# Performance work log

Measured on AMD Instinct MI355X. Metric: run time of the kernel, lower is better.

## Reference

```python
import jax, jax.numpy as jnp
import numpy as np
import math

D_MODEL, H, D_FF = 1024, 16, 4096
B, S = 4, 2048
EPS = 1e-6

def layer_norm(x, alpha, beta):
    # Faithful to torch: x.std uses Bessel correction (ddof=1), eps added to std.
    mean = jnp.mean(x, axis=-1, keepdims=True)
    std = jnp.std(x, axis=-1, keepdims=True, ddof=1)
    return alpha * (x - mean) / (std + EPS) + beta

def setup_inputs() -> dict:
    key = jax.random.key(0)
    ks = jax.random.split(key, 8)
    sc = 0.02
    return {
        "x": jax.random.normal(ks[0], (B, S, D_MODEL), jnp.float32),
        "mask": jnp.ones((B, 1, 1, S), jnp.int32),
        "wq": jax.random.normal(ks[1], (D_MODEL, D_MODEL), jnp.float32) * sc,
        "wk": jax.random.normal(ks[2], (D_MODEL, D_MODEL), jnp.float32) * sc,
        "wv": jax.random.normal(ks[3], (D_MODEL, D_MODEL), jnp.float32) * sc,
        "wo": jax.random.normal(ks[4], (D_MODEL, D_MODEL), jnp.float32) * sc,
        "w1": jax.random.normal(ks[5], (D_MODEL, D_FF), jnp.float32) * sc,
        "b1": jnp.zeros((D_FF,), jnp.float32),
        "w2": jax.random.normal(ks[6], (D_FF, D_MODEL), jnp.float32) * sc,
        "b2": jnp.zeros((D_MODEL,), jnp.float32),
        "ln1_a": jnp.ones((D_MODEL,), jnp.float32),
        "ln1_b": jnp.zeros((D_MODEL,), jnp.float32),
        "ln2_a": jnp.ones((D_MODEL,), jnp.float32),
        "ln2_b": jnp.zeros((D_MODEL,), jnp.float32),
    }

def mha(xn, mask, wq, wk, wv, wo):
    b, s, d = xn.shape
    d_k = d // H
    q = (xn @ wq).reshape(b, s, H, d_k).transpose(0, 2, 1, 3)  # [B,H,S,dk]
    k = (xn @ wk).reshape(b, s, H, d_k).transpose(0, 2, 1, 3)
    v = (xn @ wv).reshape(b, s, H, d_k).transpose(0, 2, 1, 3)
    scores = jnp.einsum('bhqd,bhkd->bhqk', q, k) / math.sqrt(d_k)
    scores = jnp.where(mask == 0, -1e9, scores)
    attn = jax.nn.softmax(scores, axis=-1)
    out = jnp.einsum('bhqk,bhkd->bhqd', attn, v)
    out = out.transpose(0, 2, 1, 3).reshape(b, s, d)
    return out @ wo

def reference(x, mask, wq, wk, wv, wo, w1, b1, w2, b2, ln1_a, ln1_b, ln2_a, ln2_b):
    # Pre-LN residual 1: self-attention (dropout=0 / eval mode -> identity)
    xn = layer_norm(x, ln1_a, ln1_b)
    x = x + mha(xn, mask, wq, wk, wv, wo)
    # Pre-LN residual 2: FFN
    xn = layer_norm(x, ln2_a, ln2_b)
    ff = jax.nn.relu(xn @ w1 + b1) @ w2 + b2
    return x + ff
```

## Files before the change

kernel.cpp:

```cpp
#include <hip/hip_runtime.h>
#include <hip/hip_bf16.h>

typedef __bf16 bf16x8 __attribute__((ext_vector_type(8)));
typedef __bf16 bf16x4 __attribute__((ext_vector_type(4)));
typedef float  f32x4  __attribute__((ext_vector_type(4)));

#define MFMA(a, b, c) __builtin_amdgcn_mfma_f32_16x16x32_bf16((a), (b), (c), 0, 0, 0)

#define GLOAD16(gp, lp) __builtin_amdgcn_global_load_lds(                      \
    (const __attribute__((address_space(1))) void*)(gp),                       \
    (__attribute__((address_space(3))) void*)(lp), 16, 0, 0)

__device__ inline unsigned int pkbf(float a, float b) {
    __bf16 x = (__bf16)a, y = (__bf16)b;
    return (unsigned int)*(unsigned short*)&x |
           ((unsigned int)*(unsigned short*)&y << 16);
}

__global__ __launch_bounds__(256) void transpose_cvt(
    const float* __restrict__ src, __bf16* __restrict__ dst, int Kd, int Nd)
{
    __shared__ float tile[32][33];
    const int k0 = blockIdx.y * 32, n0 = blockIdx.x * 32;
    const int t = threadIdx.x;
    const int r = t >> 5, c = t & 31;
#pragma unroll
    for (int i = 0; i < 4; ++i)
        tile[r + i * 8][c] = src[(long)(k0 + r + i * 8) * Nd + n0 + c];
    __syncthreads();
#pragma unroll
    for (int i = 0; i < 4; ++i)
        dst[(long)(n0 + r + i * 8) * Kd + k0 + c] = (__bf16)tile[c][r + i * 8];
}

__global__ __launch_bounds__(256) void transpose_v(
    const __bf16* __restrict__ V, __bf16* __restrict__ Vt)
{
    __shared__ __bf16 tile[32][33];
    const int bh = blockIdx.z;
    const int s0 = blockIdx.x * 32, d0 = blockIdx.y * 32;
    const int t = threadIdx.x, r = t >> 5, c = t & 31;
    const __bf16* Vp = V + (long)bh * 2048 * 64;
    __bf16* Tp = Vt + (long)bh * 64 * 2048;
#pragma unroll
    for (int i = 0; i < 4; ++i)
        tile[r + i * 8][c] = Vp[(long)(s0 + r + i * 8) * 64 + d0 + c];
    __syncthreads();
#pragma unroll
    for (int i = 0; i < 4; ++i)
        Tp[(long)(d0 + r + i * 8) * 2048 + s0 + c] = tile[c][r + i * 8];
}

__global__ __launch_bounds__(256) void ln_kernel(
    const float* __restrict__ in, const float* __restrict__ ga,
    const float* __restrict__ gb, __bf16* __restrict__ out)
{
    const int row = blockIdx.x;
    const int t = threadIdx.x;
    const float4 xv = *(const float4*)(in + (long)row * 1024 + t * 4);
    float s  = xv.x + xv.y + xv.z + xv.w;
    float sq = xv.x * xv.x + xv.y * xv.y + xv.z * xv.z + xv.w * xv.w;
#pragma unroll
    for (int off = 32; off; off >>= 1) {
        s  += __shfl_xor(s, off);
        sq += __shfl_xor(sq, off);
    }
    __shared__ float red[8];
    const int w = t >> 6;
    if ((t & 63) == 0) { red[w * 2] = s; red[w * 2 + 1] = sq; }
    __syncthreads();
    s  = red[0] + red[2] + red[4] + red[6];
    sq = red[1] + red[3] + red[5] + red[7];
    const float mean = s * (1.0f / 1024.0f);
    const float var  = fmaxf((sq - s * mean) * (1.0f / 1023.0f), 0.0f);
    const float dinv = 1.0f / (sqrtf(var) + 1e-6f);
    const float4 av = *(const float4*)(ga + t * 4);
    const float4 bv = *(const float4*)(gb + t * 4);
    bf16x4 o;
    o[0] = (__bf16)((xv.x - mean) * dinv * av.x + bv.x);
    o[1] = (__bf16)((xv.y - mean) * dinv * av.y + bv.y);
    o[2] = (__bf16)((xv.z - mean) * dinv * av.z + bv.z);
    o[3] = (__bf16)((xv.w - mean) * dinv * av.w + bv.w);
    *(bf16x4*)(out + (long)row * 1024 + t * 4) = o;
}

template <int MODE>
__global__ __launch_bounds__(512, 2) void gemm256(
    const __bf16* __restrict__ A, const __bf16* __restrict__ Bt,
    int M, int N, int K,
    const float* __restrict__ bias, __bf16* __restrict__ outb,
    __bf16* __restrict__ qb, __bf16* __restrict__ kb2, __bf16* __restrict__ vb)
{
    __shared__ __align__(16) char LDS[131072];

    const int t = threadIdx.x;
    const int lane = t & 63;
    const int g = lane >> 4, l15 = lane & 15;
    const int wid = t >> 6;
    const int wm = wid >> 2, wn = wid & 3;

    const int nwg = gridDim.x * gridDim.y;
    const int hwid = blockIdx.y * gridDim.x + blockIdx.x;
    const int swid = (hwid & 7) * (nwg >> 3) + (hwid >> 3);
    const int bm = (swid / gridDim.x) * 256;
    const int bn = (swid % gridDim.x) * 256;

    int r1, kb1, r2, kbb2;
    { const int p = t >> 3, sv = (t & 7) ^ (p & 7);
      r1 = 2 * p + ((sv >> 2) & 1); kb1 = (sv & 3) * 16; }
    { const int c = t + 512, p = c >> 3, sv = (c & 7) ^ (p & 7);
      r2 = 2 * p + ((sv >> 2) & 1); kbb2 = (sv & 3) * 16; }
    const char* a1 = (const char*)A  + ((long)(bm + r1) * K) * 2 + kb1;
    const char* a2 = (const char*)A  + ((long)(bm + r2) * K) * 2 + kbb2;
    const char* b1 = (const char*)Bt + ((long)(bn + r1) * K) * 2 + kb1;
    const char* b2 = (const char*)Bt + ((long)(bn + r2) * K) * 2 + kbb2;
    char* const dA1 = LDS + t * 16;
    char* const dA2 = LDS + 8192 + t * 16;
    char* const dB1 = LDS + 65536 + t * 16;
    char* const dB2 = LDS + 65536 + 8192 + t * 16;

#define STG(kt, kh, buf) do {                                                  \
        const long go_ = (long)(kt) * 128 + (kh) * 64;                         \
        const int lo_ = (buf) * 32768 + (kh) * 16384;                          \
        GLOAD16(a1 + go_, dA1 + lo_); GLOAD16(a2 + go_, dA2 + lo_);            \
        GLOAD16(b1 + go_, dB1 + lo_); GLOAD16(b2 + go_, dB2 + lo_); } while (0)

    const int ph = l15 >> 1;
    const int slot = ((((l15 & 1) << 2) | g) ^ ph) << 4;
    const int aoff = wm * 8192 + ph * 128 + slot;
    const int boff = 65536 + wn * 4096 + ph * 128 + slot;

    f32x4 acc[8][4] = {};
    const int nt = K / 64;

    STG(0, 0, 0);
    STG(0, 1, 0);

    for (int kt = 0; kt < nt; ++kt) {
        const int cur = kt & 1;
#pragma unroll
        for (int kh = 0; kh < 2; ++kh) {
            asm volatile("s_waitcnt vmcnt(4)" ::: "memory");
            asm volatile("s_barrier" ::: "memory");
            if (kt + 1 < nt) STG(kt + 1, kh, cur ^ 1);
            const char* pl = LDS + cur * 32768 + kh * 16384;
            bf16x8 af[8], bfr[4];
#pragma unroll
            for (int ni = 0; ni < 4; ++ni)
                bfr[ni] = *(const bf16x8*)(pl + boff + ni * 1024);
#pragma unroll
            for (int mi = 0; mi < 8; ++mi)
                af[mi] = *(const bf16x8*)(pl + aoff + mi * 1024);
            __builtin_amdgcn_s_setprio(1);
#pragma unroll
            for (int mi = 0; mi < 8; ++mi)
#pragma unroll
                for (int ni = 0; ni < 4; ++ni)
                    acc[mi][ni] = MFMA(af[mi], bfr[ni], acc[mi][ni]);
            __builtin_amdgcn_s_setprio(0);
        }
    }
#undef STG

#pragma unroll
    for (int mi = 0; mi < 8; ++mi) {
#pragma unroll
        for (int ni = 0; ni < 4; ++ni) {
#pragma unroll
            for (int r = 0; r < 4; ++r) {
                const int gr = bm + wm * 128 + mi * 16 + g * 4 + r;
                const int gc = bn + wn * 64 + ni * 16 + l15;
                const float v = acc[mi][ni][r];
                if constexpr (MODE == 0) {
                    const int bufi = gc >> 10;
                    const int hd = gc & 1023;
                    const int h = hd >> 6, d = hd & 63;
                    const int b = gr >> 11, sx = gr & 2047;
                    __bf16* dst = (bufi == 0) ? qb : ((bufi == 1) ? kb2 : vb);
                    dst[((long)((b * 16 + h) * 2048 + sx)) * 64 + d] = (__bf16)v;
                } else {
                    const float y = fmaxf(v + bias[gc], 0.0f);
                    outb[(long)gr * N + gc] = (__bf16)y;
                }
            }
        }
    }
}

template <int MODE>
__global__ __launch_bounds__(256) void gemm_bt(
    const __bf16* __restrict__ A, const __bf16* __restrict__ Bt,
    int M, int N, int K,
    const float* __restrict__ bias, const float* resid,
    float* outf, __bf16* __restrict__ outb)
{
    __shared__ __align__(16) __bf16 Alds[2][128 * 32];
    __shared__ __align__(16) __bf16 Blds[2][128 * 32];

    const int t = threadIdx.x;
    const int lane = t & 63, w = t >> 6;
    const int wr = w >> 1, wc = w & 1;
    const int g = lane >> 4, l15 = lane & 15;

    const int nwg = gridDim.x * gridDim.y;
    const int hwid = blockIdx.y * gridDim.x + blockIdx.x;
    const int wid = (hwid & 7) * (nwg >> 3) + (hwid >> 3);
    const int bm = (wid / gridDim.x) * 128;
    const int bn = (wid % gridDim.x) * 128;

    const int cr = t >> 2;
    const int cc = (t & 3) * 8;
    const __bf16* Ag  = A  + (long)(bm + cr) * K + cc;
    const __bf16* Ag2 = Ag + (long)64 * K;
    const __bf16* Bg  = Bt + (long)(bn + cr) * K + cc;
    const __bf16* Bg2 = Bg + (long)64 * K;
    const int wof = cr * 32 + cc;

    f32x4 acc[4][4] = {};
    const int nk = K / 32;

    bf16x8 ra0 = *(const bf16x8*)(Ag);
    bf16x8 ra1 = *(const bf16x8*)(Ag2);
    bf16x8 rb0 = *(const bf16x8*)(Bg);
    bf16x8 rb1 = *(const bf16x8*)(Bg2);
    *(bf16x8*)(&Alds[0][wof])           = ra0;
    *(bf16x8*)(&Alds[0][wof + 64 * 32]) = ra1;
    *(bf16x8*)(&Blds[0][wof])           = rb0;
    *(bf16x8*)(&Blds[0][wof + 64 * 32]) = rb1;
    ra0 = *(const bf16x8*)(Ag  + 32);
    ra1 = *(const bf16x8*)(Ag2 + 32);
    rb0 = *(const bf16x8*)(Bg  + 32);
    rb1 = *(const bf16x8*)(Bg2 + 32);
    __syncthreads();

    for (int kt = 0; kt < nk; ++kt) {
        const int cur = kt & 1;
        if (kt + 1 < nk) {
            *(bf16x8*)(&Alds[cur ^ 1][wof])           = ra0;
            *(bf16x8*)(&Alds[cur ^ 1][wof + 64 * 32]) = ra1;
            *(bf16x8*)(&Blds[cur ^ 1][wof])           = rb0;
            *(bf16x8*)(&Blds[cur ^ 1][wof + 64 * 32]) = rb1;
            if (kt + 2 < nk) {
                const long ko = (long)(kt + 2) * 32;
                ra0 = *(const bf16x8*)(Ag  + ko);
                ra1 = *(const bf16x8*)(Ag2 + ko);
                rb0 = *(const bf16x8*)(Bg  + ko);
                rb1 = *(const bf16x8*)(Bg2 + ko);
            }
        }
        const __bf16* Ab = &Alds[cur][0];
        const __bf16* Bb = &Blds[cur][0];
        bf16x8 af[4], bfr[4];
#pragma unroll
        for (int mi = 0; mi < 4; ++mi)
            af[mi] = *(const bf16x8*)(Ab + (wr * 64 + mi * 16 + l15) * 32 + g * 8);
#pragma unroll
        for (int ni = 0; ni < 4; ++ni)
            bfr[ni] = *(const bf16x8*)(Bb + (wc * 64 + ni * 16 + l15) * 32 + g * 8);
#pragma unroll
        for (int mi = 0; mi < 4; ++mi)
#pragma unroll
            for (int ni = 0; ni < 4; ++ni)
                acc[mi][ni] = MFMA(af[mi], bfr[ni], acc[mi][ni]);
        __syncthreads();
    }

#pragma unroll
    for (int mi = 0; mi < 4; ++mi) {
#pragma unroll
        for (int ni = 0; ni < 4; ++ni) {
#pragma unroll
            for (int r = 0; r < 4; ++r) {
                const int gr = bm + wr * 64 + mi * 16 + g * 4 + r;
                const int gc = bn + wc * 64 + ni * 16 + l15;
                const float vacc = acc[mi][ni][r];
                if constexpr (MODE == 1) {
                    const long idx = (long)gr * N + gc;
                    outf[idx] = vacc + resid[idx];
                } else {
                    const long idx = (long)gr * N + gc;
                    outf[idx] = vacc + bias[gc] + resid[idx];
                }
            }
        }
    }
}

__global__ __launch_bounds__(256, 2) void attn_kernel(
    const __bf16* __restrict__ Q, const __bf16* __restrict__ Kk,
    const __bf16* __restrict__ Vt, const int* __restrict__ mask,
    __bf16* __restrict__ O)
{
    __shared__ __align__(16) char Klds[8192];
    __shared__ __align__(16) char Vlds[8192];
    __shared__ int mlds[64];
    __shared__ int tflag[32];

    const int t = threadIdx.x;
    const int lane = t & 63, w = t >> 6;
    const int g = lane >> 4, l15 = lane & 15;
    const int bh = blockIdx.x >> 4;
    const int qt = blockIdx.x & 15;
    const int b = bh >> 4, h = bh & 15;
    const int q0 = qt * 128 + w * 32;

    const __bf16* Qp = Q  + (long)bh * 2048 * 64;
    const __bf16* Kp = Kk + (long)bh * 2048 * 64;
    const __bf16* Vp = Vt + (long)bh * 64 * 2048;
    const int* mp = mask + b * 2048;

    {
        const int4* mi4 = (const int4*)(mp + t * 8);
        const int4 ma = mi4[0], mb = mi4[1];
        const int ok = (ma.x && ma.y && ma.z && ma.w &&
                        mb.x && mb.y && mb.z && mb.w) ? 1 : 0;
        const unsigned long long bal = __ballot(ok);
        if ((lane & 7) == 0)
            tflag[t >> 3] = (((bal >> lane) & 0xFFull) == 0xFFull) ? 1 : 0;
    }

    bf16x8 qreg[2][2];
#pragma unroll
    for (int qf = 0; qf < 2; ++qf)
#pragma unroll
        for (int kh = 0; kh < 2; ++kh)
            qreg[qf][kh] = *(const bf16x8*)(Qp + (long)(q0 + qf * 16 + l15) * 64 + kh * 32 + g * 8);

    bf16x8 vone;
#pragma unroll
    for (int j = 0; j < 8; ++j) vone[j] = (__bf16)1.0f;

    const float Csc = 0.18033688011112042f;
    float m2_run[2] = {-1e30f, -1e30f};
    f32x4 la[2] = {};
    f32x4 ot[2][4] = {};

    const int sr0 = t >> 3;
    const int sce = (t & 7) * 8;
    const int swz0 = sr0 * 128 + (((t & 7) * 16) ^ ((sr0 & 7) << 4));
    const int swz1 = swz0 + 32 * 128;

    bf16x8 kr0 = *(const bf16x8*)(Kp + (long)sr0 * 64 + sce);
    bf16x8 kr1 = *(const bf16x8*)(Kp + (long)(sr0 + 32) * 64 + sce);
    bf16x8 vr0 = *(const bf16x8*)(Vp + (long)sr0 * 2048 + sce);
    bf16x8 vr1 = *(const bf16x8*)(Vp + (long)(sr0 + 32) * 2048 + sce);
    int mr = (t < 64) ? mp[t] : 0;

    for (int kc = 0; kc < 32; ++kc) {
        __syncthreads();
        *(bf16x8*)(Klds + swz0) = kr0;
        *(bf16x8*)(Klds + swz1) = kr1;
        *(bf16x8*)(Vlds + swz0) = vr0;
        *(bf16x8*)(Vlds + swz1) = vr1;
        if (t < 64) mlds[t] = mr;
        __syncthreads();
        if (kc < 31) {
            const int kv0 = (kc + 1) * 64;
            kr0 = *(const bf16x8*)(Kp + (long)(kv0 + sr0) * 64 + sce);
            kr1 = *(const bf16x8*)(Kp + (long)(kv0 + sr0 + 32) * 64 + sce);
            vr0 = *(const bf16x8*)(Vp + (long)sr0 * 2048 + kv0 + sce);
            vr1 = *(const bf16x8*)(Vp + (long)(sr0 + 32) * 2048 + kv0 + sce);
            if (t < 64) mr = mp[kv0 + t];
        }
        const bool fullv = (tflag[kc] != 0);

        bf16x8 kf[4][2];
#pragma unroll
        for (int f = 0; f < 4; ++f)
#pragma unroll
            for (int dh = 0; dh < 2; ++dh)
                kf[f][dh] = *(const bf16x8*)(Klds + (f * 16 + l15) * 128 +
                                             ((dh * 64 + g * 16) ^ ((l15 & 7) << 4)));
        f32x4 sf[2][4] = {};
        __builtin_amdgcn_s_setprio(1);
#pragma unroll
        for (int qf = 0; qf < 2; ++qf)
#pragma unroll
            for (int f = 0; f < 4; ++f) {
                sf[qf][f] = MFMA(kf[f][0], qreg[qf][0], sf[qf][f]);
                sf[qf][f] = MFMA(kf[f][1], qreg[qf][1], sf[qf][f]);
            }
        __builtin_amdgcn_s_setprio(0);

        bf16x8 av[4][2];
#pragma unroll
        for (int df = 0; df < 4; ++df) {
            const int row = (df * 16 + l15) * 128;
            const int sx = (l15 & 7) << 4;
#pragma unroll
            for (int hh = 0; hh < 2; ++hh) {
                const bf16x4 lo = *(const bf16x4*)(Vlds + row + ((hh * 64 + g * 8) ^ sx));
                const bf16x4 hi = *(const bf16x4*)(Vlds + row + ((hh * 64 + 32 + g * 8) ^ sx));
                bf16x8 a;
                a[0] = lo[0]; a[1] = lo[1]; a[2] = lo[2]; a[3] = lo[3];
                a[4] = hi[0]; a[5] = hi[1]; a[6] = hi[2]; a[7] = hi[3];
                av[df][hh] = a;
            }
        }

#pragma unroll
        for (int qf = 0; qf < 2; ++qf) {
            float s[16];
            if (fullv) {
#pragma unroll
                for (int i = 0; i < 16; ++i) s[i] = sf[qf][i >> 2][i & 3];
            } else {
                int mvv[16];
#pragma unroll
                for (int f = 0; f < 4; ++f) {
                    const int4 mq = *(const int4*)&mlds[f * 16 + g * 4];
                    mvv[f * 4 + 0] = mq.x; mvv[f * 4 + 1] = mq.y;
                    mvv[f * 4 + 2] = mq.z; mvv[f * 4 + 3] = mq.w;
                }
#pragma unroll
                for (int i = 0; i < 16; ++i)
                    s[i] = (mvv[i] == 0) ? -1e9f : sf[qf][i >> 2][i & 3];
            }
            float m01 = fmaxf(s[0], s[1]),   m23 = fmaxf(s[2], s[3]);
            float m45 = fmaxf(s[4], s[5]),   m67 = fmaxf(s[6], s[7]);
            float m89 = fmaxf(s[8], s[9]),   mab = fmaxf(s[10], s[11]);
            float mcd = fmaxf(s[12], s[13]), mef = fmaxf(s[14], s[15]);
            float mx = fmaxf(fmaxf(fmaxf(m01, m23), fmaxf(m45, m67)),
                             fmaxf(fmaxf(m89, mab), fmaxf(mcd, mef)));
            mx = fmaxf(mx, __shfl_xor(mx, 16));
            mx = fmaxf(mx, __shfl_xor(mx, 32));
            const float m2 = mx * Csc;
            if (!__all(m2 - m2_run[qf] <= 8.0f)) {
                const float m2n = fmaxf(m2_run[qf], m2);
                const float alpha = __builtin_amdgcn_exp2f(m2_run[qf] - m2n);
#pragma unroll
                for (int r = 0; r < 4; ++r) la[qf][r] *= alpha;
#pragma unroll
                for (int df = 0; df < 4; ++df)
#pragma unroll
                    for (int r = 0; r < 4; ++r) ot[qf][df][r] *= alpha;
                m2_run[qf] = m2n;
            }
            const float nm2 = -m2_run[qf];
            float p[16];
#pragma unroll
            for (int i = 0; i < 16; ++i)
                p[i] = __builtin_amdgcn_exp2f(__builtin_fmaf(s[i], Csc, nm2));

#pragma unroll
            for (int hh = 0; hh < 2; ++hh) {
                unsigned int pu[4] = {pkbf(p[hh * 8 + 0], p[hh * 8 + 1]),
                                      pkbf(p[hh * 8 + 2], p[hh * 8 + 3]),
                                      pkbf(p[hh * 8 + 4], p[hh * 8 + 5]),
                                      pkbf(p[hh * 8 + 6], p[hh * 8 + 7])};
                bf16x8 pf = *(bf16x8*)pu;
                __builtin_amdgcn_s_setprio(1);
#pragma unroll
                for (int df = 0; df < 4; ++df)
                    ot[qf][df] = MFMA(av[df][hh], pf, ot[qf][df]);
                la[qf] = MFMA(vone, pf, la[qf]);
                __builtin_amdgcn_s_setprio(0);
            }
        }
    }

#pragma unroll
    for (int qf = 0; qf < 2; ++qf) {
        const float inv = 1.0f / la[qf][0];
        const int q = q0 + qf * 16 + l15;
        __bf16* orow = O + (long)(b * 2048 + q) * 1024 + h * 64;
#pragma unroll
        for (int df = 0; df < 4; ++df)
#pragma unroll
            for (int rp = 0; rp < 2; ++rp) {
                const int d = df * 16 + g * 4 + rp * 2;
                *(unsigned int*)(orow + d) =
                    pkbf(ot[qf][df][rp * 2] * inv, ot[qf][df][rp * 2 + 1] * inv);
            }
    }
}

extern "C" void kernel_launch(void* const* d_in, const int* in_sizes, int n_in,
                              void* d_out, int out_size, void* d_ws, size_t ws_size,
                              hipStream_t stream)
{
    const float* x    = (const float*)d_in[0];
    const int*   mask = (const int*)  d_in[1];
    const float* wq   = (const float*)d_in[2];
    const float* wk   = (const float*)d_in[3];
    const float* wv   = (const float*)d_in[4];
    const float* wo   = (const float*)d_in[5];
    const float* w1   = (const float*)d_in[6];
    const float* b1   = (const float*)d_in[7];
    const float* w2   = (const float*)d_in[8];
    const float* b2   = (const float*)d_in[9];
    const float* l1a  = (const float*)d_in[10];
    const float* l1b  = (const float*)d_in[11];
    const float* l2a  = (const float*)d_in[12];
    const float* l2b  = (const float*)d_in[13];
    float* out = (float*)d_out;

    char* ws = (char*)d_ws;
    __bf16* wqkvT = (__bf16*)(ws);
    __bf16* woT   = (__bf16*)(ws + 6291456);
    __bf16* w1T   = (__bf16*)(ws + 8388608);
    __bf16* w2T   = (__bf16*)(ws + 16777216);
    __bf16* xn    = (__bf16*)(ws + 25165824);
    __bf16* Vtb   = (__bf16*)(ws + 25165824);
    __bf16* Qb    = (__bf16*)(ws + 41943040);
    __bf16* Kb    = (__bf16*)(ws + 58720256);
    __bf16* Vb    = (__bf16*)(ws + 75497472);
    __bf16* attO  = (__bf16*)(ws + 92274688);
    __bf16* ffh   = (__bf16*)(ws + 41943040);

    transpose_cvt<<<dim3(32, 32),  256, 0, stream>>>(wq, wqkvT,               1024, 1024);
    transpose_cvt<<<dim3(32, 32),  256, 0, stream>>>(wk, wqkvT + 1024 * 1024, 1024, 1024);
    transpose_cvt<<<dim3(32, 32),  256, 0, stream>>>(wv, wqkvT + 2048 * 1024, 1024, 1024);
    transpose_cvt<<<dim3(32, 32),  256, 0, stream>>>(wo, woT,                 1024, 1024);
    transpose_cvt<<<dim3(128, 32), 256, 0, stream>>>(w1, w1T,                 1024, 4096);
    transpose_cvt<<<dim3(32, 128), 256, 0, stream>>>(w2, w2T,                 4096, 1024);

    ln_kernel<<<8192, 256, 0, stream>>>(x, l1a, l1b, xn);
    gemm256<0><<<dim3(12, 32), 512, 0, stream>>>(xn, wqkvT, 8192, 3072, 1024,
                                                 nullptr, nullptr, Qb, Kb, Vb);
    transpose_v<<<dim3(64, 2, 64), 256, 0, stream>>>(Vb, Vtb);
    attn_kernel<<<1024, 256, 0, stream>>>(Qb, Kb, Vtb, mask, attO);
    gemm_bt<1><<<dim3(8, 64), 256, 0, stream>>>(attO, woT, 8192, 1024, 1024,
                                                nullptr, x, out, nullptr);
    ln_kernel<<<8192, 256, 0, stream>>>(out, l2a, l2b, xn);
    gemm256<2><<<dim3(16, 32), 512, 0, stream>>>(xn, w1T, 8192, 4096, 1024,
                                                 b1, ffh, nullptr, nullptr, nullptr);
    gemm_bt<3><<<dim3(8, 64), 256, 0, stream>>>(ffh, w2T, 8192, 1024, 4096,
                                                b2, out, out, nullptr);
    (void)in_sizes; (void)n_in; (void)out_size; (void)ws_size;
}
```

Before: 462.0 us.

## Split GEMM k-step into two half phases interleaving A/B prefetch with MFMA

Restructures the GEMM main loop so each k-half runs in two phases. Each phase loads four A fragments, issues half of the next-tile global-to-LDS prefetch (A first, then B), and runs sixteen MFMAs, with barriers between phases. The aim is to spread global load issue across the MFMA work and cut register pressure from holding eight A fragments at once. In exchange it adds extra barriers per k-half and changes the vmcnt waits at the last iteration.

```diff
diff --git a/kernel.cpp b/kernel.cpp
--- a/kernel.cpp
+++ b/kernel.cpp
@@ -119,10 +119,13 @@
     char* const dB1 = LDS + 65536 + t * 16;
     char* const dB2 = LDS + 65536 + 8192 + t * 16;
 
-#define STG(kt, kh, buf) do {                                                  \
+#define STG_A(kt, kh, buf) do {                                                \
         const long go_ = (long)(kt) * 128 + (kh) * 64;                         \
         const int lo_ = (buf) * 32768 + (kh) * 16384;                          \
-        GLOAD16(a1 + go_, dA1 + lo_); GLOAD16(a2 + go_, dA2 + lo_);            \
+        GLOAD16(a1 + go_, dA1 + lo_); GLOAD16(a2 + go_, dA2 + lo_); } while (0)
+#define STG_B(kt, kh, buf) do {                                                \
+        const long go_ = (long)(kt) * 128 + (kh) * 64;                         \
+        const int lo_ = (buf) * 32768 + (kh) * 16384;                          \
         GLOAD16(b1 + go_, dB1 + lo_); GLOAD16(b2 + go_, dB2 + lo_); } while (0)
 
     const int ph = l15 >> 1;
@@ -133,34 +136,52 @@
     f32x4 acc[8][4] = {};
     const int nt = K / 64;
 
-    STG(0, 0, 0);
-    STG(0, 1, 0);
+    STG_A(0, 0, 0); STG_B(0, 0, 0); STG_A(0, 1, 0); STG_B(0, 1, 0);
 
     for (int kt = 0; kt < nt; ++kt) {
         const int cur = kt & 1;
+        const bool pre = (kt + 1 < nt);
 #pragma unroll
         for (int kh = 0; kh < 2; ++kh) {
-            asm volatile("s_waitcnt vmcnt(4)" ::: "memory");
-            asm volatile("s_barrier" ::: "memory");
-            if (kt + 1 < nt) STG(kt + 1, kh, cur ^ 1);
             const char* pl = LDS + cur * 32768 + kh * 16384;
-            bf16x8 af[8], bfr[4];
+            if (kh == 0 || pre) {
+                asm volatile("s_waitcnt vmcnt(4)" ::: "memory");
+            } else {
+                asm volatile("s_waitcnt vmcnt(0)" ::: "memory");
+            }
+            __builtin_amdgcn_s_barrier();
+            bf16x8 bfr[4], af[4];
 #pragma unroll
             for (int ni = 0; ni < 4; ++ni)
                 bfr[ni] = *(const bf16x8*)(pl + boff + ni * 1024);
 #pragma unroll
-            for (int mi = 0; mi < 8; ++mi)
+            for (int mi = 0; mi < 4; ++mi)
                 af[mi] = *(const bf16x8*)(pl + aoff + mi * 1024);
+            if (pre) STG_A(kt + 1, kh, cur ^ 1);
             __builtin_amdgcn_s_setprio(1);
 #pragma unroll
-            for (int mi = 0; mi < 8; ++mi)
+            for (int mi = 0; mi < 4; ++mi)
 #pragma unroll
                 for (int ni = 0; ni < 4; ++ni)
                     acc[mi][ni] = MFMA(af[mi], bfr[ni], acc[mi][ni]);
             __builtin_amdgcn_s_setprio(0);
-        }
-    }
-#undef STG
+            __builtin_amdgcn_s_barrier();
+#pragma unroll
+            for (int mi = 0; mi < 4; ++mi)
+                af[mi] = *(const bf16x8*)(pl + aoff + (mi + 4) * 1024);
+            if (pre) STG_B(kt + 1, kh, cur ^ 1);
+            __builtin_amdgcn_s_setprio(1);
+#pragma unroll
+            for (int mi = 0; mi < 4; ++mi)
+#pragma unroll
+                for (int ni = 0; ni < 4; ++ni)
+                    acc[mi + 4][ni] = MFMA(af[mi], bfr[ni], acc[mi + 4][ni]);
+            __builtin_amdgcn_s_setprio(0);
+            __builtin_amdgcn_s_barrier();
+        }
+    }
+#undef STG_A
+#undef STG_B
 
 #pragma unroll
     for (int mi = 0; mi < 8; ++mi) {
```

Measured after the change: 460.6 us. No clear change (-0.3%).
